# Kernel optimization log

Hardware: AMD Instinct MI355X
Metric: run time of the kernel (lower is better)

The kernel has to match this reference:

```python
import jax, jax.numpy as jnp
import numpy as np


def setup_inputs() -> dict:
    key = jax.random.key(0)
    k0, k1, k2, k3 = jax.random.split(key, 4)
    B, N, C = 4, 1024, 64
    x = jax.random.normal(k0, (B, N, C), dtype=jnp.float32)
    # torch nn.Linear weights are [out, in]; all projections are bias-free
    W1 = jax.random.normal(k1, (C, C), dtype=jnp.float32) * (1.0 / np.sqrt(C))
    W2 = jax.random.normal(k2, (C, C), dtype=jnp.float32) * (1.0 / np.sqrt(C))
    w3 = jax.random.normal(k3, (C,), dtype=jnp.float32) * (1.0 / np.sqrt(C))
    return {"x": x, "W1": W1, "W2": W2, "w3": w3}


def reference(x, W1, W2, w3):
    # x: [B, N, C]; torch Linear: y = x @ W.T
    x1 = jnp.einsum("bnc,dc->bnd", x, W1)  # [B, N, C]
    x2 = jnp.einsum("bnc,dc->bnd", x, W2)  # [B, N, C]
    # broadcast-add over node pairs, tanh, project C -> 1: [B, N, N]
    combined = jnp.tanh(x1[:, :, None, :] + x2[:, None, :, :])  # [B, N, N, C]
    att = jnp.einsum("bijc,c->bij", combined, w3)
    return jax.nn.softmax(att, axis=-1)
```

## Files before the change

kernel.cpp:

```cpp
#include <hip/hip_runtime.h>
#include <hip/hip_bf16.h>


#define BATCH 4
#define NN    1024
#define CC    64
#define TI    4
#define BLK   256
#define NCH   (NN / BLK)

__device__ __forceinline__ float fast_exp2(float x) {
#if __has_builtin(__builtin_amdgcn_exp2f)
    return __builtin_amdgcn_exp2f(x);
#else
    return exp2f(x);
#endif
}
__device__ __forceinline__ float fast_rcp(float x) {
#if __has_builtin(__builtin_amdgcn_rcpf)
    return __builtin_amdgcn_rcpf(x);
#else
    return 1.0f / x;
#endif
}

__global__ __launch_bounds__(256) void proj_kernel(
    const float* __restrict__ x, const float* __restrict__ W1,
    const float* __restrict__ W2, float* __restrict__ e1p,
    float* __restrict__ e2p) {
    const int w    = threadIdx.x >> 6;
    const int lane = threadIdx.x & 63;
    const int r    = blockIdx.x * 4 + w;
    const float4* __restrict__ xrow  = (const float4*)(x  + (size_t)r    * CC);
    const float4* __restrict__ w1row = (const float4*)(W1 + (size_t)lane * CC);
    const float4* __restrict__ w2row = (const float4*)(W2 + (size_t)lane * CC);
    float a1 = 0.f, a2 = 0.f;
#pragma unroll
    for (int q = 0; q < 16; ++q) {
        float4 xv = xrow[q];
        float4 u  = w1row[q];
        float4 v  = w2row[q];
        a1 = fmaf(xv.x, u.x, a1); a1 = fmaf(xv.y, u.y, a1);
        a1 = fmaf(xv.z, u.z, a1); a1 = fmaf(xv.w, u.w, a1);
        a2 = fmaf(xv.x, v.x, a2); a2 = fmaf(xv.y, v.y, a2);
        a2 = fmaf(xv.z, v.z, a2); a2 = fmaf(xv.w, v.w, a2);
    }
    const float K2 = 2.8853900817779268f;
    e1p[(size_t)r * CC + lane] = fast_exp2(fminf(a1 * K2, 15.f));
    e2p[(size_t)r * CC + lane] = fast_exp2(fminf(a2 * K2, 15.f));
}

__global__ __launch_bounds__(BLK) void attn_kernel(
    const float* __restrict__ e1p, const float* __restrict__ e2p,
    const float* __restrict__ w3, float* __restrict__ out) {
    __shared__ float e1t[CC * TI];
    __shared__ float w3s[CC];
    __shared__ float att_lds[TI * NN];

    const int tid = threadIdx.x;
    const int bi  = blockIdx.x;
    const int b   = bi >> 8;
    const int i0  = (bi & 255) * TI;

    {
        const int ii = tid >> 6, c = tid & 63;
        e1t[c * TI + ii] = e1p[(size_t)((b << 10) + i0 + ii) * CC + c];
        if (tid < CC) w3s[tid] = w3[tid];
    }
    __syncthreads();

    float sumw3 = 0.f;
#pragma unroll
    for (int c = 0; c < CC; ++c) sumw3 += w3s[c];

    const float4* __restrict__ e2r =
        (const float4*)(e2p + ((size_t)b << 10) * CC);
    const float4* e1t4 = (const float4*)e1t;
    const float4* w3s4 = (const float4*)w3s;

    for (int ch = 0; ch < NCH; ++ch) {
        const int j = ch * BLK + tid;
        const float4* __restrict__ row = e2r + (size_t)j * 16;

        float acc0 = 0.f, acc1 = 0.f, acc2 = 0.f, acc3 = 0.f;
        auto step = [&](const float4 a, const float ec, const float wc) {
            acc0 = fmaf(wc, fast_rcp(fmaf(a.x, ec, 1.f)), acc0);
            acc1 = fmaf(wc, fast_rcp(fmaf(a.y, ec, 1.f)), acc1);
            acc2 = fmaf(wc, fast_rcp(fmaf(a.z, ec, 1.f)), acc2);
            acc3 = fmaf(wc, fast_rcp(fmaf(a.w, ec, 1.f)), acc3);
        };
#pragma unroll 1
        for (int ct = 0; ct < 4; ++ct) {
            float4 e2q0 = row[ct * 4 + 0];
            float4 e2q1 = row[ct * 4 + 1];
            float4 e2q2 = row[ct * 4 + 2];
            float4 e2q3 = row[ct * 4 + 3];
            const int q0 = ct * 4;
            float4 wq0 = w3s4[q0 + 0], wq1 = w3s4[q0 + 1];
            float4 wq2 = w3s4[q0 + 2], wq3 = w3s4[q0 + 3];
            step(e1t4[4 * (q0 + 0) + 0], e2q0.x, wq0.x);
            step(e1t4[4 * (q0 + 0) + 1], e2q0.y, wq0.y);
            step(e1t4[4 * (q0 + 0) + 2], e2q0.z, wq0.z);
            step(e1t4[4 * (q0 + 0) + 3], e2q0.w, wq0.w);
            step(e1t4[4 * (q0 + 1) + 0], e2q1.x, wq1.x);
            step(e1t4[4 * (q0 + 1) + 1], e2q1.y, wq1.y);
            step(e1t4[4 * (q0 + 1) + 2], e2q1.z, wq1.z);
            step(e1t4[4 * (q0 + 1) + 3], e2q1.w, wq1.w);
            step(e1t4[4 * (q0 + 2) + 0], e2q2.x, wq2.x);
            step(e1t4[4 * (q0 + 2) + 1], e2q2.y, wq2.y);
            step(e1t4[4 * (q0 + 2) + 2], e2q2.z, wq2.z);
            step(e1t4[4 * (q0 + 2) + 3], e2q2.w, wq2.w);
            step(e1t4[4 * (q0 + 3) + 0], e2q3.x, wq3.x);
            step(e1t4[4 * (q0 + 3) + 1], e2q3.y, wq3.y);
            step(e1t4[4 * (q0 + 3) + 2], e2q3.z, wq3.z);
            step(e1t4[4 * (q0 + 3) + 3], e2q3.w, wq3.w);
        }
        att_lds[0 * NN + j] = fmaf(-2.f, acc0, sumw3);
        att_lds[1 * NN + j] = fmaf(-2.f, acc1, sumw3);
        att_lds[2 * NN + j] = fmaf(-2.f, acc2, sumw3);
        att_lds[3 * NN + j] = fmaf(-2.f, acc3, sumw3);
    }
    __syncthreads();

    {
        const int w    = tid >> 6;
        const int lane = tid & 63;
        float v[16];
        float m = -3.4e38f;
#pragma unroll
        for (int k = 0; k < 16; ++k) {
            v[k] = att_lds[w * NN + k * 64 + lane];
            m = fmaxf(m, v[k]);
        }
#pragma unroll
        for (int off = 32; off >= 1; off >>= 1)
            m = fmaxf(m, __shfl_xor(m, off));
        const float L2E = 1.4426950408889634f;
        float s = 0.f;
#pragma unroll
        for (int k = 0; k < 16; ++k) {
            v[k] = fast_exp2((v[k] - m) * L2E);
            s += v[k];
        }
#pragma unroll
        for (int off = 32; off >= 1; off >>= 1)
            s += __shfl_xor(s, off);
        const float rs = fast_rcp(s);
        float* __restrict__ orow = out + (((size_t)(b << 10) + (i0 + w)) << 10);
#pragma unroll
        for (int k = 0; k < 16; ++k) orow[k * 64 + lane] = v[k] * rs;
    }
}

extern "C" void kernel_launch(void* const* d_in, const int* in_sizes, int n_in,
                              void* d_out, int out_size, void* d_ws, size_t ws_size,
                              hipStream_t stream) {
    const float* x  = (const float*)d_in[0];
    const float* W1 = (const float*)d_in[1];
    const float* W2 = (const float*)d_in[2];
    const float* w3 = (const float*)d_in[3];
    float* outp = (float*)d_out;

    float* e1p = (float*)d_ws;
    float* e2p = e1p + (size_t)BATCH * NN * CC;

    proj_kernel<<<dim3(BATCH * NN / 4), dim3(256), 0, stream>>>(x, W1, W2, e1p, e2p);
    attn_kernel<<<dim3(BATCH * NN / TI), dim3(BLK), 0, stream>>>(e1p, e2p, w3, outp);
}
```

Measured before the change: 115.6 us.

## Pair reciprocals to halve rcp count, process two j rows per thread, stage weights in LDS

The attention inner loop now computes two tanh-reciprocals with a single rcp on the product of the denominators, trading one transcendental for extra multiplies. Each thread handles two j rows per chunk so each e1 LDS read is reused across more pairs. w3 is read straight from global memory instead of LDS. The projection kernel stages transposed W1/W2 in padded LDS to avoid strided global reads. Multiplying two denominators can overflow when both are large (up to exp2(15) each), which risks inf/precision issues.

New measurement: 104.4 us. 1.11x faster.

```diff
diff --git a/kernel.cpp b/kernel.cpp
--- a/kernel.cpp
+++ b/kernel.cpp
@@ -7,7 +7,9 @@
 #define CC    64
 #define TI    4
 #define BLK   256
-#define NCH   (NN / BLK)
+#define J2    2
+#define NCH   (NN / (BLK * J2))
+#define PP    65
 
 __device__ __forceinline__ float fast_exp2(float x) {
 #if __has_builtin(__builtin_amdgcn_exp2f)
@@ -28,33 +30,62 @@
     const float* __restrict__ x, const float* __restrict__ W1,
     const float* __restrict__ W2, float* __restrict__ e1p,
     float* __restrict__ e2p) {
-    const int w    = threadIdx.x >> 6;
-    const int lane = threadIdx.x & 63;
+    __shared__ float w1t[CC * PP];
+    __shared__ float w2t[CC * PP];
+
+    const int tid = threadIdx.x;
+    {
+        const float4* __restrict__ W1v = (const float4*)W1;
+        const float4* __restrict__ W2v = (const float4*)W2;
+#pragma unroll
+        for (int k = 0; k < 4; ++k) {
+            const int fi = k * 256 + tid;
+            const int r  = fi >> 4;
+            const int c4 = (fi & 15) * 4;
+            float4 a = W1v[fi], b = W2v[fi];
+            w1t[(c4 + 0) * PP + r] = a.x; w1t[(c4 + 1) * PP + r] = a.y;
+            w1t[(c4 + 2) * PP + r] = a.z; w1t[(c4 + 3) * PP + r] = a.w;
+            w2t[(c4 + 0) * PP + r] = b.x; w2t[(c4 + 1) * PP + r] = b.y;
+            w2t[(c4 + 2) * PP + r] = b.z; w2t[(c4 + 3) * PP + r] = b.w;
+        }
+    }
+    __syncthreads();
+
+    const int w    = tid >> 6;
+    const int lane = tid & 63;
     const int r    = blockIdx.x * 4 + w;
-    const float4* __restrict__ xrow  = (const float4*)(x  + (size_t)r    * CC);
-    const float4* __restrict__ w1row = (const float4*)(W1 + (size_t)lane * CC);
-    const float4* __restrict__ w2row = (const float4*)(W2 + (size_t)lane * CC);
+    const float4* __restrict__ xr = (const float4*)(x + (size_t)r * CC);
+
     float a1 = 0.f, a2 = 0.f;
 #pragma unroll
     for (int q = 0; q < 16; ++q) {
-        float4 xv = xrow[q];
-        float4 u  = w1row[q];
-        float4 v  = w2row[q];
-        a1 = fmaf(xv.x, u.x, a1); a1 = fmaf(xv.y, u.y, a1);
-        a1 = fmaf(xv.z, u.z, a1); a1 = fmaf(xv.w, u.w, a1);
-        a2 = fmaf(xv.x, v.x, a2); a2 = fmaf(xv.y, v.y, a2);
-        a2 = fmaf(xv.z, v.z, a2); a2 = fmaf(xv.w, v.w, a2);
+        const float4 xv = xr[q];
+        const float xc[4] = {xv.x, xv.y, xv.z, xv.w};
+#pragma unroll
+        for (int m = 0; m < 4; ++m) {
+            const int c = 4 * q + m;
+            a1 = fmaf(xc[m], w1t[c * PP + lane], a1);
+            a2 = fmaf(xc[m], w2t[c * PP + lane], a2);
+        }
     }
     const float K2 = 2.8853900817779268f;
     e1p[(size_t)r * CC + lane] = fast_exp2(fminf(a1 * K2, 15.f));
     e2p[(size_t)r * CC + lane] = fast_exp2(fminf(a2 * K2, 15.f));
 }
 
+__device__ __forceinline__ void step2(float e1a, float e1b, float e2,
+                                      float wc, float2& acc) {
+    float da = fmaf(e1a, e2, 1.f);
+    float db = fmaf(e1b, e2, 1.f);
+    float r  = fast_rcp(da * db);
+    acc.x = fmaf(wc * db, r, acc.x);
+    acc.y = fmaf(wc * da, r, acc.y);
+}
+
 __global__ __launch_bounds__(BLK) void attn_kernel(
     const float* __restrict__ e1p, const float* __restrict__ e2p,
     const float* __restrict__ w3, float* __restrict__ out) {
     __shared__ float e1t[CC * TI];
-    __shared__ float w3s[CC];
     __shared__ float att_lds[TI * NN];
 
     const int tid = threadIdx.x;
@@ -65,60 +96,59 @@
     {
         const int ii = tid >> 6, c = tid & 63;
         e1t[c * TI + ii] = e1p[(size_t)((b << 10) + i0 + ii) * CC + c];
-        if (tid < CC) w3s[tid] = w3[tid];
     }
     __syncthreads();
 
+    const float4* __restrict__ w3q = (const float4*)w3;
     float sumw3 = 0.f;
 #pragma unroll
-    for (int c = 0; c < CC; ++c) sumw3 += w3s[c];
+    for (int q = 0; q < 16; ++q) {
+        float4 t = w3q[q];
+        sumw3 += (t.x + t.y) + (t.z + t.w);
+    }
 
-    const float4* __restrict__ e2r =
-        (const float4*)(e2p + ((size_t)b << 10) * CC);
+    const float* __restrict__ e2b = e2p + ((size_t)b << 10) * CC;
     const float4* e1t4 = (const float4*)e1t;
-    const float4* w3s4 = (const float4*)w3s;
 
+#pragma unroll 1
     for (int ch = 0; ch < NCH; ++ch) {
-        const int j = ch * BLK + tid;
-        const float4* __restrict__ row = e2r + (size_t)j * 16;
+        const int j0 = ch * (BLK * J2) + tid;
+        const float4* __restrict__ rowA = (const float4*)(e2b + (size_t)j0 * CC);
+        const float4* __restrict__ rowB = rowA + (BLK * CC / 4);
 
-        float acc0 = 0.f, acc1 = 0.f, acc2 = 0.f, acc3 = 0.f;
-        auto step = [&](const float4 a, const float ec, const float wc) {
-            acc0 = fmaf(wc, fast_rcp(fmaf(a.x, ec, 1.f)), acc0);
-            acc1 = fmaf(wc, fast_rcp(fmaf(a.y, ec, 1.f)), acc1);
-            acc2 = fmaf(wc, fast_rcp(fmaf(a.z, ec, 1.f)), acc2);
-            acc3 = fmaf(wc, fast_rcp(fmaf(a.w, ec, 1.f)), acc3);
-        };
+        float2 accA0 = {0.f, 0.f}, accA1 = {0.f, 0.f};
+        float2 accB0 = {0.f, 0.f}, accB1 = {0.f, 0.f};
+
 #pragma unroll 1
         for (int ct = 0; ct < 4; ++ct) {
-            float4 e2q0 = row[ct * 4 + 0];
-            float4 e2q1 = row[ct * 4 + 1];
-            float4 e2q2 = row[ct * 4 + 2];
-            float4 e2q3 = row[ct * 4 + 3];
-            const int q0 = ct * 4;
-            float4 wq0 = w3s4[q0 + 0], wq1 = w3s4[q0 + 1];
-            float4 wq2 = w3s4[q0 + 2], wq3 = w3s4[q0 + 3];
-            step(e1t4[4 * (q0 + 0) + 0], e2q0.x, wq0.x);
-            step(e1t4[4 * (q0 + 0) + 1], e2q0.y, wq0.y);
-            step(e1t4[4 * (q0 + 0) + 2], e2q0.z, wq0.z);
-            step(e1t4[4 * (q0 + 0) + 3], e2q0.w, wq0.w);
-            step(e1t4[4 * (q0 + 1) + 0], e2q1.x, wq1.x);
-            step(e1t4[4 * (q0 + 1) + 1], e2q1.y, wq1.y);
-            step(e1t4[4 * (q0 + 1) + 2], e2q1.z, wq1.z);
-            step(e1t4[4 * (q0 + 1) + 3], e2q1.w, wq1.w);
-            step(e1t4[4 * (q0 + 2) + 0], e2q2.x, wq2.x);
-            step(e1t4[4 * (q0 + 2) + 1], e2q2.y, wq2.y);
-            step(e1t4[4 * (q0 + 2) + 2], e2q2.z, wq2.z);
-            step(e1t4[4 * (q0 + 2) + 3], e2q2.w, wq2.w);
-            step(e1t4[4 * (q0 + 3) + 0], e2q3.x, wq3.x);
-            step(e1t4[4 * (q0 + 3) + 1], e2q3.y, wq3.y);
-            step(e1t4[4 * (q0 + 3) + 2], e2q3.z, wq3.z);
-            step(e1t4[4 * (q0 + 3) + 3], e2q3.w, wq3.w);
+#pragma unroll
+            for (int q = 0; q < 4; ++q) {
+                const float4 eAv = rowA[ct * 4 + q];
+                const float4 eBv = rowB[ct * 4 + q];
+                const float4 wv  = w3q[ct * 4 + q];
+                const float eAa[4] = {eAv.x, eAv.y, eAv.z, eAv.w};
+                const float eBa[4] = {eBv.x, eBv.y, eBv.z, eBv.w};
+                const float wa[4]  = {wv.x, wv.y, wv.z, wv.w};
+#pragma unroll
+                for (int m = 0; m < 4; ++m) {
+                    const int c = ct * 16 + q * 4 + m;
+                    const float4 ev = e1t4[c];
+                    step2(ev.x, ev.y, eAa[m], wa[m], accA0);
+                    step2(ev.z, ev.w, eAa[m], wa[m], accA1);
+                    step2(ev.x, ev.y, eBa[m], wa[m], accB0);
+                    step2(ev.z, ev.w, eBa[m], wa[m], accB1);
+                }
+            }
         }
-        att_lds[0 * NN + j] = fmaf(-2.f, acc0, sumw3);
-        att_lds[1 * NN + j] = fmaf(-2.f, acc1, sumw3);
-        att_lds[2 * NN + j] = fmaf(-2.f, acc2, sumw3);
-        att_lds[3 * NN + j] = fmaf(-2.f, acc3, sumw3);
+        const int j1 = j0 + BLK;
+        att_lds[0 * NN + j0] = fmaf(-2.f, accA0.x, sumw3);
+        att_lds[1 * NN + j0] = fmaf(-2.f, accA0.y, sumw3);
+        att_lds[2 * NN + j0] = fmaf(-2.f, accA1.x, sumw3);
+        att_lds[3 * NN + j0] = fmaf(-2.f, accA1.y, sumw3);
+        att_lds[0 * NN + j1] = fmaf(-2.f, accB0.x, sumw3);
+        att_lds[1 * NN + j1] = fmaf(-2.f, accB0.y, sumw3);
+        att_lds[2 * NN + j1] = fmaf(-2.f, accB1.x, sumw3);
+        att_lds[3 * NN + j1] = fmaf(-2.f, accB1.y, sumw3);
     }
     __syncthreads();
 
```
